# Optimization experiments

Hardware: AMD Instinct MI355X
Metric: run time of the kernel (lower is better)

## Reference

```python
import jax, jax.numpy as jnp
from jax import lax
import numpy as np

B, C, H, W = 32, 256, 56, 56
G1, G2 = 64, 4          # groups for 3x3 convs, number of parallel convs / 1x1 groups
EPS = 1e-5
DN = ('NCHW', 'OIHW', 'NCHW')


def setup_inputs() -> dict:
    key = jax.random.key(0)
    it = iter(jax.random.split(key, 32))
    nk = lambda: next(it)
    n = lambda shape, s=0.05: jax.random.normal(nk(), shape, jnp.float32) * s
    u = lambda shape: jax.random.uniform(nk(), shape, jnp.float32, minval=0.5, maxval=1.5)
    inp = {'x': jax.random.normal(nk(), (B, C, H, W), jnp.float32)}
    inp.update(
        w1=n((G2, G1, C // G1, 3, 3), 0.1), b1=n((G2, G1)),
        bn1a_g=1.0 + n((C,)), bn1a_b=n((C,)), bn1a_m=n((C,)), bn1a_v=u((C,)),
        pw1=n((C, C // G2, 1, 1), 0.1), pb1=n((C,)),
        bn1b_g=1.0 + n((C,)), bn1b_b=n((C,)), bn1b_m=n((C,)), bn1b_v=u((C,)),
        w2=n((G2, G1, C // G1, 3, 3), 0.1), b2=n((G2, G1)),
        bn2a_g=1.0 + n((C,)), bn2a_b=n((C,)), bn2a_m=n((C,)), bn2a_v=u((C,)),
        pw2=n((C, C // G2, 1, 1), 0.1), pb2=n((C,)),
        bn2b_g=1.0 + n((C,)), bn2b_b=n((C,)), bn2b_m=n((C,)), bn2b_v=u((C,)),
    )
    return inp


def _bn_relu(x, g, b, m, v):
    # inference-mode BatchNorm2d + ReLU, fused into one affine + relu
    inv = g / jnp.sqrt(v + EPS)
    return jax.nn.relu(x * inv[None, :, None, None] + (b - m * inv)[None, :, None, None])


def _gconv3x3(x, w, b):
    # Faithful to: [Conv2d(Cin, g1, k=3, p=1, groups=g1) for _ in range(g2)] then concat(dim=1).
    # Implemented as ONE grouped conv (feature_group_count=g1) followed by a cheap channel permute
    # to recover torch's concat ordering (conv-index major, group minor).
    g2, g1, cpg = w.shape[0], w.shape[1], w.shape[2]
    # combined weight: out channel k*g2 + i (group-major) uses conv i, group k
    Wc = jnp.transpose(w, (1, 0, 2, 3, 4)).reshape(g1 * g2, cpg, 3, 3)
    y = lax.conv_general_dilated(x, Wc, (1, 1), ((1, 1), (1, 1)),
                                 feature_group_count=g1, dimension_numbers=DN)
    Bx, _, Hy, Wy = y.shape
    # (g, i) ordering -> torch concat (i, g) ordering
    y = y.reshape(Bx, g1, g2, Hy, Wy).transpose(0, 2, 1, 3, 4).reshape(Bx, g1 * g2, Hy, Wy)
    return y + b.reshape(g1 * g2)[None, :, None, None]


def _pwconv(x, w, b):
    # Conv2d(C, C, k=1, groups=G2)
    y = lax.conv_general_dilated(x, w, (1, 1), 'VALID',
                                 feature_group_count=G2, dimension_numbers=DN)
    return y + b[None, :, None, None]


def reference(x, w1, b1, bn1a_g, bn1a_b, bn1a_m, bn1a_v, pw1, pb1,
              bn1b_g, bn1b_b, bn1b_m, bn1b_v,
              w2, b2, bn2a_g, bn2a_b, bn2a_m, bn2a_v, pw2, pb2,
              bn2b_g, bn2b_b, bn2b_m, bn2b_v):
    h = _gconv3x3(x, w1, b1)
    h = _bn_relu(h, bn1a_g, bn1a_b, bn1a_m, bn1a_v)
    h = _pwconv(h, pw1, pb1)
    h = _bn_relu(h, bn1b_g, bn1b_b, bn1b_m, bn1b_v)
    h = _gconv3x3(h, w2, b2)
    h = _bn_relu(h, bn2a_g, bn2a_b, bn2a_m, bn2a_v)
    h = _pwconv(h, pw2, pb2)
    h = _bn_relu(h, bn2b_g, bn2b_b, bn2b_m, bn2b_v)
    return h
```

## Files before the change

### kernel.cpp

```cpp
#include <hip/hip_runtime.h>

#define HW 3136
#define SHS 232

__global__ __launch_bounds__(256, 2) void fused_stage(
    const float* __restrict__ in,
    const float* __restrict__ gw,
    const float* __restrict__ gb,
    const float* __restrict__ bnag, const float* __restrict__ bnab,
    const float* __restrict__ bnam, const float* __restrict__ bnav,
    const float* __restrict__ pw,
    const float* __restrict__ pb,
    const float* __restrict__ bnbg, const float* __restrict__ bnbb,
    const float* __restrict__ bnbm, const float* __restrict__ bnbv,
    float* __restrict__ out)
{
    __shared__ float sH[64 * SHS];
    __shared__ float sW[64 * 64];

    const int tid = threadIdx.x;
    const int blk = blockIdx.x;
    const int t   = blk % 14;
    const int g   = (blk / 14) & 3;
    const int b   = blk / 56;
    const int y0  = t * 4;

    {
        const int o  = tid & 63;
        const int c0 = (tid >> 6) * 16;
        const float* src = pw + (size_t)(g * 64 + o) * 64 + c0;
        float4 v0 = *(const float4*)(src + 0);
        float4 v1 = *(const float4*)(src + 4);
        float4 v2 = *(const float4*)(src + 8);
        float4 v3 = *(const float4*)(src + 12);
        float tmp[16] = {v0.x, v0.y, v0.z, v0.w, v1.x, v1.y, v1.z, v1.w,
                         v2.x, v2.y, v2.z, v2.w, v3.x, v3.y, v3.z, v3.w};
#pragma unroll
        for (int j = 0; j < 16; ++j)
            sW[(c0 + j) * 64 + o] = tmp[j];
    }

    const int k  = tid >> 2;
    const int xs = tid & 3;
    const int x0 = xs * 14;

    float wr[36];
    {
        const float4* w4 = (const float4*)(gw + (size_t)(g * 64 + k) * 36);
#pragma unroll
        for (int j = 0; j < 9; ++j) {
            float4 v = w4[j];
            wr[4*j+0] = v.x; wr[4*j+1] = v.y; wr[4*j+2] = v.z; wr[4*j+3] = v.w;
        }
    }

    float acc[4][14];
#pragma unroll
    for (int r = 0; r < 4; ++r)
#pragma unroll
        for (int xx = 0; xx < 14; ++xx) acc[r][xx] = 0.f;

#pragma unroll
    for (int cc = 0; cc < 4; ++cc) {
        const float* chp = in + ((size_t)(b * 256 + k * 4 + cc)) * HW;
#pragma unroll
        for (int ry = 0; ry < 6; ++ry) {
            const int gy = y0 - 1 + ry;
            if ((unsigned)gy >= 56u) continue;
            const float* rp = chp + gy * 56;
            float rr[16];
            rr[0]  = (x0 > 0)       ? rp[x0 - 1]  : 0.f;
            rr[15] = (x0 + 14 < 56) ? rp[x0 + 14] : 0.f;
#pragma unroll
            for (int j = 0; j < 7; ++j) {
                float2 v = *(const float2*)(rp + x0 + 2 * j);
                rr[1 + 2*j] = v.x; rr[2 + 2*j] = v.y;
            }
            const int rlo = (ry >= 2) ? ry - 2 : 0;
            const int rhi = (ry <= 3) ? ry : 3;
#pragma unroll
            for (int r = 0; r < 4; ++r) {
                if (r < rlo || r > rhi) continue;
                const int dy = ry - r;
                const float w0 = wr[cc*9 + dy*3 + 0];
                const float w1 = wr[cc*9 + dy*3 + 1];
                const float w2 = wr[cc*9 + dy*3 + 2];
#pragma unroll
                for (int xx = 0; xx < 14; ++xx)
                    acc[r][xx] = fmaf(w2, rr[xx+2],
                                 fmaf(w1, rr[xx+1],
                                 fmaf(w0, rr[xx], acc[r][xx])));
            }
        }
    }

    {
        const int c = g * 64 + k;
        const float sc = bnag[c] * rsqrtf(bnav[c] + 1e-5f);
        const float sh = fmaf(gb[c], sc, bnab[c] - bnam[c] * sc);
#pragma unroll
        for (int r = 0; r < 4; ++r)
#pragma unroll
            for (int j = 0; j < 7; ++j) {
                float v0 = fmaxf(fmaf(acc[r][2*j],   sc, sh), 0.f);
                float v1 = fmaxf(fmaf(acc[r][2*j+1], sc, sh), 0.f);
                *(float2*)&sH[k * SHS + r * 56 + x0 + 2*j] = make_float2(v0, v1);
            }
    }
    __syncthreads();

    const int og = tid >> 4;
    const int pg = tid & 15;
    const int p0 = pg * 14;

    float a2[4][14];
#pragma unroll
    for (int i = 0; i < 4; ++i)
#pragma unroll
        for (int xx = 0; xx < 14; ++xx) a2[i][xx] = 0.f;

    for (int c = 0; c < 64; ++c) {
        const float4 wv = *(const float4*)&sW[c * 64 + og * 4];
        float hr[14];
#pragma unroll
        for (int j = 0; j < 7; ++j) {
            float2 v = *(const float2*)&sH[c * SHS + p0 + 2*j];
            hr[2*j] = v.x; hr[2*j+1] = v.y;
        }
#pragma unroll
        for (int xx = 0; xx < 14; ++xx) {
            a2[0][xx] = fmaf(wv.x, hr[xx], a2[0][xx]);
            a2[1][xx] = fmaf(wv.y, hr[xx], a2[1][xx]);
            a2[2][xx] = fmaf(wv.z, hr[xx], a2[2][xx]);
            a2[3][xx] = fmaf(wv.w, hr[xx], a2[3][xx]);
        }
    }

#pragma unroll
    for (int i = 0; i < 4; ++i) {
        const int o = g * 64 + og * 4 + i;
        const float sc = bnbg[o] * rsqrtf(bnbv[o] + 1e-5f);
        const float sh = fmaf(pb[o], sc, bnbb[o] - bnbm[o] * sc);
        float* op = out + ((size_t)(b * 256 + o)) * HW + y0 * 56 + p0;
#pragma unroll
        for (int j = 0; j < 7; ++j) {
            float v0 = fmaxf(fmaf(a2[i][2*j],   sc, sh), 0.f);
            float v1 = fmaxf(fmaf(a2[i][2*j+1], sc, sh), 0.f);
            *(float2*)(op + 2*j) = make_float2(v0, v1);
        }
    }
}

extern "C" void kernel_launch(void* const* d_in, const int* in_sizes, int n_in,
                              void* d_out, int out_size, void* d_ws, size_t ws_size,
                              hipStream_t stream) {
    const float* x     = (const float*)d_in[0];
    const float* w1    = (const float*)d_in[1];
    const float* b1    = (const float*)d_in[2];
    const float* bn1ag = (const float*)d_in[3];
    const float* bn1ab = (const float*)d_in[4];
    const float* bn1am = (const float*)d_in[5];
    const float* bn1av = (const float*)d_in[6];
    const float* pw1   = (const float*)d_in[7];
    const float* pb1   = (const float*)d_in[8];
    const float* bn1bg = (const float*)d_in[9];
    const float* bn1bb = (const float*)d_in[10];
    const float* bn1bm = (const float*)d_in[11];
    const float* bn1bv = (const float*)d_in[12];
    const float* w2    = (const float*)d_in[13];
    const float* b2    = (const float*)d_in[14];
    const float* bn2ag = (const float*)d_in[15];
    const float* bn2ab = (const float*)d_in[16];
    const float* bn2am = (const float*)d_in[17];
    const float* bn2av = (const float*)d_in[18];
    const float* pw2   = (const float*)d_in[19];
    const float* pb2   = (const float*)d_in[20];
    const float* bn2bg = (const float*)d_in[21];
    const float* bn2bb = (const float*)d_in[22];
    const float* bn2bm = (const float*)d_in[23];
    const float* bn2bv = (const float*)d_in[24];

    float* mid  = (float*)d_ws;
    float* outp = (float*)d_out;

    const int grid = 32 * 4 * 14;

    fused_stage<<<grid, 256, 0, stream>>>(x,   w1, b1, bn1ag, bn1ab, bn1am, bn1av,
                                          pw1, pb1, bn1bg, bn1bb, bn1bm, bn1bv, mid);
    fused_stage<<<grid, 256, 0, stream>>>(mid, w2, b2, bn2ag, bn2ab, bn2am, bn2av,
                                          pw2, pb2, bn2bg, bn2bb, bn2bm, bn2bv, outp);
}
```

Baseline: 475.6 us.

## Halve row tile, drop shared pointwise weights, remap blocks for XCD locality

Each block now computes 2 output rows instead of 4, which doubles the grid and shrinks shared memory and registers so more blocks fit per CU (launch bounds raised to 5). The 1x1 weights are read directly from global memory as float4s instead of being staged in LDS. Block indices are remapped so that the four channel groups of the same batch/tile land on the same XCD, sharing input rows in L2. The trade-off is more halo re-reads of input rows (4 rows loaded per 2 output rows) and global weight loads inside the pointwise loop.

```diff
diff --git a/kernel.cpp b/kernel.cpp
--- a/kernel.cpp
+++ b/kernel.cpp
@@ -1,9 +1,9 @@
 #include <hip/hip_runtime.h>
 
 #define HW 3136
-#define SHS 232
+#define SHS 120
 
-__global__ __launch_bounds__(256, 2) void fused_stage(
+__global__ __launch_bounds__(256, 5) void fused_stage(
     const float* __restrict__ in,
     const float* __restrict__ gw,
     const float* __restrict__ gb,
@@ -16,55 +16,39 @@
     float* __restrict__ out)
 {
     __shared__ float sH[64 * SHS];
-    __shared__ float sW[64 * 64];
 
     const int tid = threadIdx.x;
-    const int blk = blockIdx.x;
-    const int t   = blk % 14;
-    const int g   = (blk / 14) & 3;
-    const int b   = blk / 56;
-    const int y0  = t * 4;
 
-    {
-        const int o  = tid & 63;
-        const int c0 = (tid >> 6) * 16;
-        const float* src = pw + (size_t)(g * 64 + o) * 64 + c0;
-        float4 v0 = *(const float4*)(src + 0);
-        float4 v1 = *(const float4*)(src + 4);
-        float4 v2 = *(const float4*)(src + 8);
-        float4 v3 = *(const float4*)(src + 12);
-        float tmp[16] = {v0.x, v0.y, v0.z, v0.w, v1.x, v1.y, v1.z, v1.w,
-                         v2.x, v2.y, v2.z, v2.w, v3.x, v3.y, v3.z, v3.w};
-#pragma unroll
-        for (int j = 0; j < 16; ++j)
-            sW[(c0 + j) * 64 + o] = tmp[j];
-    }
+    const int idx  = blockIdx.x;
+    const int xcd  = idx & 7;
+    const int qq   = idx >> 3;
+    const int g    = qq & 3;
+    const int slot = qq >> 2;
+    const int u    = slot * 8 + xcd;
+    const int b    = u / 28;
+    const int t    = u - b * 28;
+    const int y0   = t * 2;
 
     const int k  = tid >> 2;
     const int xs = tid & 3;
     const int x0 = xs * 14;
 
-    float wr[36];
-    {
-        const float4* w4 = (const float4*)(gw + (size_t)(g * 64 + k) * 36);
+    float acc[2][14];
 #pragma unroll
-        for (int j = 0; j < 9; ++j) {
-            float4 v = w4[j];
-            wr[4*j+0] = v.x; wr[4*j+1] = v.y; wr[4*j+2] = v.z; wr[4*j+3] = v.w;
-        }
-    }
-
-    float acc[4][14];
-#pragma unroll
-    for (int r = 0; r < 4; ++r)
+    for (int r = 0; r < 2; ++r)
 #pragma unroll
         for (int xx = 0; xx < 14; ++xx) acc[r][xx] = 0.f;
 
+    const float* wkp = gw + (size_t)(g * 64 + k) * 36;
+
 #pragma unroll
     for (int cc = 0; cc < 4; ++cc) {
+        float wr9[9];
+#pragma unroll
+        for (int j = 0; j < 9; ++j) wr9[j] = wkp[cc * 9 + j];
         const float* chp = in + ((size_t)(b * 256 + k * 4 + cc)) * HW;
 #pragma unroll
-        for (int ry = 0; ry < 6; ++ry) {
+        for (int ry = 0; ry < 4; ++ry) {
             const int gy = y0 - 1 + ry;
             if ((unsigned)gy >= 56u) continue;
             const float* rp = chp + gy * 56;
@@ -76,15 +60,13 @@
                 float2 v = *(const float2*)(rp + x0 + 2 * j);
                 rr[1 + 2*j] = v.x; rr[2 + 2*j] = v.y;
             }
-            const int rlo = (ry >= 2) ? ry - 2 : 0;
-            const int rhi = (ry <= 3) ? ry : 3;
 #pragma unroll
-            for (int r = 0; r < 4; ++r) {
-                if (r < rlo || r > rhi) continue;
-                const int dy = ry - r;
-                const float w0 = wr[cc*9 + dy*3 + 0];
-                const float w1 = wr[cc*9 + dy*3 + 1];
-                const float w2 = wr[cc*9 + dy*3 + 2];
+            for (int r = 0; r < 2; ++r) {
+                const int wi = ry - r;
+                if (wi < 0 || wi > 2) continue;
+                const float w0 = wr9[wi*3 + 0];
+                const float w1 = wr9[wi*3 + 1];
+                const float w2 = wr9[wi*3 + 2];
 #pragma unroll
                 for (int xx = 0; xx < 14; ++xx)
                     acc[r][xx] = fmaf(w2, rr[xx+2],
@@ -99,7 +81,7 @@
         const float sc = bnag[c] * rsqrtf(bnav[c] + 1e-5f);
         const float sh = fmaf(gb[c], sc, bnab[c] - bnam[c] * sc);
 #pragma unroll
-        for (int r = 0; r < 4; ++r)
+        for (int r = 0; r < 2; ++r)
 #pragma unroll
             for (int j = 0; j < 7; ++j) {
                 float v0 = fmaxf(fmaf(acc[r][2*j],   sc, sh), 0.f);
@@ -109,39 +91,50 @@
     }
     __syncthreads();
 
-    const int og = tid >> 4;
-    const int pg = tid & 15;
+    const int og = tid >> 3;
+    const int pg = tid & 7;
     const int p0 = pg * 14;
 
-    float a2[4][14];
+    float a2[2][14];
 #pragma unroll
-    for (int i = 0; i < 4; ++i)
+    for (int i = 0; i < 2; ++i)
 #pragma unroll
         for (int xx = 0; xx < 14; ++xx) a2[i][xx] = 0.f;
 
-    for (int c = 0; c < 64; ++c) {
-        const float4 wv = *(const float4*)&sW[c * 64 + og * 4];
-        float hr[14];
+    const float* wp0 = pw + (size_t)(g * 64 + og * 2) * 64;
+
+#pragma unroll 2
+    for (int c = 0; c < 64; c += 4) {
+        const float4 w0 = *(const float4*)(wp0 + c);
+        const float4 w1 = *(const float4*)(wp0 + 64 + c);
+        const float w0a[4] = {w0.x, w0.y, w0.z, w0.w};
+        const float w1a[4] = {w1.x, w1.y, w1.z, w1.w};
 #pragma unroll
-        for (int j = 0; j < 7; ++j) {
-            float2 v = *(const float2*)&sH[c * SHS + p0 + 2*j];
-            hr[2*j] = v.x; hr[2*j+1] = v.y;
-        }
+        for (int q2 = 0; q2 < 4; ++q2) {
+            float hr[14];
 #pragma unroll
-        for (int xx = 0; xx < 14; ++xx) {
-            a2[0][xx] = fmaf(wv.x, hr[xx], a2[0][xx]);
-            a2[1][xx] = fmaf(wv.y, hr[xx], a2[1][xx]);
-            a2[2][xx] = fmaf(wv.z, hr[xx], a2[2][xx]);
-            a2[3][xx] = fmaf(wv.w, hr[xx], a2[3][xx]);
+            for (int j = 0; j < 7; ++j) {
+                float2 v = *(const float2*)&sH[(c + q2) * SHS + p0 + 2*j];
+                hr[2*j] = v.x; hr[2*j+1] = v.y;
+            }
+            const float wa = w0a[q2];
+            const float wb = w1a[q2];
+#pragma unroll
+            for (int xx = 0; xx < 14; ++xx) {
+                a2[0][xx] = fmaf(wa, hr[xx], a2[0][xx]);
+                a2[1][xx] = fmaf(wb, hr[xx], a2[1][xx]);
+            }
         }
     }
 
+    const int orow = y0 + ((p0 >= 56) ? 1 : 0);
+    const int ox   = (p0 >= 56) ? p0 - 56 : p0;
 #pragma unroll
-    for (int i = 0; i < 4; ++i) {
-        const int o = g * 64 + og * 4 + i;
+    for (int i = 0; i < 2; ++i) {
+        const int o = g * 64 + og * 2 + i;
         const float sc = bnbg[o] * rsqrtf(bnbv[o] + 1e-5f);
         const float sh = fmaf(pb[o], sc, bnbb[o] - bnbm[o] * sc);
-        float* op = out + ((size_t)(b * 256 + o)) * HW + y0 * 56 + p0;
+        float* op = out + ((size_t)(b * 256 + o)) * HW + orow * 56 + ox;
 #pragma unroll
         for (int j = 0; j < 7; ++j) {
             float v0 = fmaxf(fmaf(a2[i][2*j],   sc, sh), 0.f);
@@ -183,7 +176,7 @@
     float* mid  = (float*)d_ws;
     float* outp = (float*)d_out;
 
-    const int grid = 32 * 4 * 14;
+    const int grid = 32 * 4 * 28;
 
     fused_stage<<<grid, 256, 0, stream>>>(x,   w1, b1, bn1ag, bn1ab, bn1am, bn1av,
                                           pw1, pb1, bn1bg, bn1bb, bn1bm, bn1bv, mid);
```

Measured after the change: 496.6 us. 4.4% more time.

## Remap blocks across XCDs, use lane shuffles for halos, read pointwise weights from global

Applied to the files above, without the earlier changes.

Block indices are remapped so that consecutive blocks, which the hardware spreads round-robin over the 8 XCDs, handle the four channel groups of the same image tile on one XCD. The aim is to share input rows in that XCD's L2. The left and right halo pixels of the 3x3 conv now come from neighbouring lanes through shuffles instead of extra scalar global loads. The pointwise weights are no longer staged in shared memory. Each thread reads float4 rows straight from global memory (cached), which removes the LDS transpose and cuts LDS usage, at the cost of more global and L1 weight traffic inside the inner loop.

```diff
diff --git a/kernel.cpp b/kernel.cpp
--- a/kernel.cpp
+++ b/kernel.cpp
@@ -16,29 +16,18 @@
     float* __restrict__ out)
 {
     __shared__ float sH[64 * SHS];
-    __shared__ float sW[64 * 64];
 
     const int tid = threadIdx.x;
-    const int blk = blockIdx.x;
-    const int t   = blk % 14;
-    const int g   = (blk / 14) & 3;
-    const int b   = blk / 56;
-    const int y0  = t * 4;
 
-    {
-        const int o  = tid & 63;
-        const int c0 = (tid >> 6) * 16;
-        const float* src = pw + (size_t)(g * 64 + o) * 64 + c0;
-        float4 v0 = *(const float4*)(src + 0);
-        float4 v1 = *(const float4*)(src + 4);
-        float4 v2 = *(const float4*)(src + 8);
-        float4 v3 = *(const float4*)(src + 12);
-        float tmp[16] = {v0.x, v0.y, v0.z, v0.w, v1.x, v1.y, v1.z, v1.w,
-                         v2.x, v2.y, v2.z, v2.w, v3.x, v3.y, v3.z, v3.w};
-#pragma unroll
-        for (int j = 0; j < 16; ++j)
-            sW[(c0 + j) * 64 + o] = tmp[j];
-    }
+    const int idx  = blockIdx.x;
+    const int xcd  = idx & 7;
+    const int qq   = idx >> 3;
+    const int g    = qq & 3;
+    const int slot = qq >> 2;
+    const int u    = slot * 8 + xcd;
+    const int b    = u / 14;
+    const int t    = u - b * 14;
+    const int y0   = t * 4;
 
     const int k  = tid >> 2;
     const int xs = tid & 3;
@@ -69,13 +58,15 @@
             if ((unsigned)gy >= 56u) continue;
             const float* rp = chp + gy * 56;
             float rr[16];
-            rr[0]  = (x0 > 0)       ? rp[x0 - 1]  : 0.f;
-            rr[15] = (x0 + 14 < 56) ? rp[x0 + 14] : 0.f;
 #pragma unroll
             for (int j = 0; j < 7; ++j) {
                 float2 v = *(const float2*)(rp + x0 + 2 * j);
                 rr[1 + 2*j] = v.x; rr[2 + 2*j] = v.y;
             }
+            const float left  = __shfl_up(rr[14], 1);
+            const float right = __shfl_down(rr[1], 1);
+            rr[0]  = (xs == 0) ? 0.f : left;
+            rr[15] = (xs == 3) ? 0.f : right;
             const int rlo = (ry >= 2) ? ry - 2 : 0;
             const int rhi = (ry <= 3) ? ry : 3;
 #pragma unroll
@@ -119,20 +110,34 @@
 #pragma unroll
         for (int xx = 0; xx < 14; ++xx) a2[i][xx] = 0.f;
 
-    for (int c = 0; c < 64; ++c) {
-        const float4 wv = *(const float4*)&sW[c * 64 + og * 4];
-        float hr[14];
+    const float* wp = pw + (size_t)(g * 64 + og * 4) * 64;
+
+    for (int c4 = 0; c4 < 64; c4 += 4) {
+        const float4 wv0 = *(const float4*)(wp + 0 * 64 + c4);
+        const float4 wv1 = *(const float4*)(wp + 1 * 64 + c4);
+        const float4 wv2 = *(const float4*)(wp + 2 * 64 + c4);
+        const float4 wv3 = *(const float4*)(wp + 3 * 64 + c4);
+        const float w0a[4] = {wv0.x, wv0.y, wv0.z, wv0.w};
+        const float w1a[4] = {wv1.x, wv1.y, wv1.z, wv1.w};
+        const float w2a[4] = {wv2.x, wv2.y, wv2.z, wv2.w};
+        const float w3a[4] = {wv3.x, wv3.y, wv3.z, wv3.w};
 #pragma unroll
-        for (int j = 0; j < 7; ++j) {
-            float2 v = *(const float2*)&sH[c * SHS + p0 + 2*j];
-            hr[2*j] = v.x; hr[2*j+1] = v.y;
-        }
+        for (int q2 = 0; q2 < 4; ++q2) {
+            const float* hrow = &sH[(c4 + q2) * SHS + p0];
+            float hr[14];
 #pragma unroll
-        for (int xx = 0; xx < 14; ++xx) {
-            a2[0][xx] = fmaf(wv.x, hr[xx], a2[0][xx]);
-            a2[1][xx] = fmaf(wv.y, hr[xx], a2[1][xx]);
-            a2[2][xx] = fmaf(wv.z, hr[xx], a2[2][xx]);
-            a2[3][xx] = fmaf(wv.w, hr[xx], a2[3][xx]);
+            for (int j = 0; j < 7; ++j) {
+                float2 v = *(const float2*)&hrow[2*j];
+                hr[2*j] = v.x; hr[2*j+1] = v.y;
+            }
+            const float wa = w0a[q2], wb = w1a[q2], wc = w2a[q2], wd = w3a[q2];
+#pragma unroll
+            for (int xx = 0; xx < 14; ++xx) {
+                a2[0][xx] = fmaf(wa, hr[xx], a2[0][xx]);
+                a2[1][xx] = fmaf(wb, hr[xx], a2[1][xx]);
+                a2[2][xx] = fmaf(wc, hr[xx], a2[2][xx]);
+                a2[3][xx] = fmaf(wd, hr[xx], a2[3][xx]);
+            }
         }
     }
 
```

Result: faster. 417.4 us (-12.2%).
